# Kernel tuning notes

Measured on AMD Instinct MI355X. Metric: run time of the kernel, lower is better.

## Reference

```python
import jax, jax.numpy as jnp
import numpy as np

EMB = 1024
HEADS = 16
HEAD_DIM = EMB // HEADS
HIDDEN = 4096
EPS = 1e-05


def setup_inputs() -> dict:
    key = jax.random.key(0)
    ks = jax.random.split(key, 12)
    B, S = 2, 2048
    s_e = 1.0 / np.sqrt(EMB)
    s_h = 1.0 / np.sqrt(HIDDEN)
    return {
        "x": jax.random.normal(ks[0], (B, S, EMB), dtype=jnp.float32),
        "Wq": jax.random.normal(ks[1], (EMB, EMB), dtype=jnp.float32) * s_e,
        "Wk": jax.random.normal(ks[2], (EMB, EMB), dtype=jnp.float32) * s_e,
        "Wv": jax.random.normal(ks[3], (EMB, EMB), dtype=jnp.float32) * s_e,
        "Wo": jax.random.normal(ks[4], (EMB, EMB), dtype=jnp.float32) * s_e,
        "bo": jnp.zeros((EMB,), dtype=jnp.float32),
        "ln1_w": jnp.ones((EMB,), dtype=jnp.float32),
        "ln1_b": jnp.zeros((EMB,), dtype=jnp.float32),
        "ln2_w": jnp.ones((EMB,), dtype=jnp.float32),
        "ln2_b": jnp.zeros((EMB,), dtype=jnp.float32),
        "W1": jax.random.normal(ks[5], (EMB, HIDDEN), dtype=jnp.float32) * s_e,
        "b1": jnp.zeros((HIDDEN,), dtype=jnp.float32),
        "W2": jax.random.normal(ks[6], (HIDDEN, EMB), dtype=jnp.float32) * s_h,
        "b2": jnp.zeros((EMB,), dtype=jnp.float32),
    }


def _layernorm(x, w, b):
    mean = jnp.mean(x, axis=-1, keepdims=True)
    var = jnp.mean(jnp.square(x - mean), axis=-1, keepdims=True)
    return (x - mean) / jnp.sqrt(var + EPS) * w + b


def _attention(x, Wq, Wk, Wv, Wo, bo):
    B, S, E = x.shape
    # project and split heads: [B, H, S, D]
    def split(h):
        return h.reshape(B, S, HEADS, HEAD_DIM).transpose(0, 2, 1, 3)
    q = split(x @ Wq)
    k = split(x @ Wk)
    v = split(x @ Wv)
    scale = 1.0 / np.sqrt(HEAD_DIM)
    scores = jnp.einsum("bhqd,bhkd->bhqk", q, k) * scale
    causal = jnp.tril(jnp.ones((S, S), dtype=bool))
    scores = jnp.where(causal[None, None], scores, -jnp.inf)
    attn = jax.nn.softmax(scores, axis=-1)
    out = jnp.einsum("bhqk,bhkd->bhqd", attn, v)
    out = out.transpose(0, 2, 1, 3).reshape(B, S, E)
    return out @ Wo + bo


def reference(x, Wq, Wk, Wv, Wo, bo, ln1_w, ln1_b, ln2_w, ln2_b, W1, b1, W2, b2):
    h = x + _attention(_layernorm(x, ln1_w, ln1_b), Wq, Wk, Wv, Wo, bo)
    ff = jax.nn.relu(_layernorm(h, ln2_w, ln2_b) @ W1 + b1) @ W2 + b2
    return h + ff
```

## Files before the change

kernel.cpp:

```cpp
#include <hip/hip_runtime.h>

typedef unsigned short u16;
typedef unsigned int u32;
typedef __attribute__((ext_vector_type(8))) short s8v;
typedef __attribute__((ext_vector_type(4))) float f4v;

#define EMB 1024
#define SEQ 2048
#define BATCH 2
#define HEADS 16
#define HDIM 64
#define HID 4096
#define MROWS 4096

__device__ __forceinline__ float bf2f(u16 h) {
    u32 u = ((u32)h) << 16;
    union { u32 u; float f; } v; v.u = u; return v.f;
}
__device__ __forceinline__ u16 f2bf(float f) {
    union { float f; u32 u; } v; v.f = f;
    u32 r = v.u + 0x7FFFu + ((v.u >> 16) & 1u);
    return (u16)(r >> 16);
}
__device__ __forceinline__ float fexp2(float x) {
    float r; asm("v_exp_f32 %0, %1" : "=v"(r) : "v"(x)); return r;
}
__device__ __forceinline__ u32 cvtpk_bf16(float lo, float hi) {
    u32 r; asm("v_cvt_pk_bf16_f32 %0, %1, %2" : "=v"(r) : "v"(lo), "v"(hi)); return r;
}

__device__ __forceinline__ void gload16(const void* g, void* l) {
    __builtin_amdgcn_global_load_lds(
        (const __attribute__((address_space(1))) unsigned int*)g,
        (__attribute__((address_space(3))) unsigned int*)l, 16, 0, 0);
}

__global__ __launch_bounds__(256) void transpose_cast(const float* __restrict__ W,
                                                      u16* __restrict__ WT, int K, int N) {
    __shared__ float tile[32][33];
    int n0 = blockIdx.x * 32, k0 = blockIdx.y * 32;
    int tx = threadIdx.x, ty = threadIdx.y;
#pragma unroll
    for (int i = ty; i < 32; i += 8)
        tile[i][tx] = W[(size_t)(k0 + i) * N + n0 + tx];
    __syncthreads();
#pragma unroll
    for (int i = ty; i < 32; i += 8)
        WT[(size_t)(n0 + i) * K + k0 + tx] = f2bf(tile[tx][i]);
}

__global__ __launch_bounds__(256) void ln_kernel(const float* __restrict__ in,
                                                 const float* __restrict__ w,
                                                 const float* __restrict__ b,
                                                 u16* __restrict__ out) {
    const int row = blockIdx.x, t = threadIdx.x;
    const float4* rp = (const float4*)(in + (size_t)row * EMB);
    float4 v = rp[t];
    float s = v.x + v.y + v.z + v.w;
    __shared__ float red[4];
#pragma unroll
    for (int off = 32; off; off >>= 1) s += __shfl_xor(s, off);
    if ((t & 63) == 0) red[t >> 6] = s;
    __syncthreads();
    float mean = (red[0] + red[1] + red[2] + red[3]) * (1.f / EMB);
    float dx = v.x - mean, dy = v.y - mean, dz = v.z - mean, dw = v.w - mean;
    float ss = dx * dx + dy * dy + dz * dz + dw * dw;
#pragma unroll
    for (int off = 32; off; off >>= 1) ss += __shfl_xor(ss, off);
    __syncthreads();
    if ((t & 63) == 0) red[t >> 6] = ss;
    __syncthreads();
    float var = (red[0] + red[1] + red[2] + red[3]) * (1.f / EMB);
    float rstd = rsqrtf(var + 1e-5f);
    float4 wv = ((const float4*)w)[t];
    float4 bv = ((const float4*)b)[t];
    u16* op = out + (size_t)row * EMB + t * 4;
    op[0] = f2bf(dx * rstd * wv.x + bv.x);
    op[1] = f2bf(dy * rstd * wv.y + bv.y);
    op[2] = f2bf(dz * rstd * wv.z + bv.z);
    op[3] = f2bf(dw * rstd * wv.w + bv.w);
}

template <int EPI, int TM, int TN, int BK>
__global__ __launch_bounds__(256) void gemm_bt(const u16* __restrict__ A, const u16* __restrict__ BT,
                                               const float* __restrict__ bias, const float* res,
                                               void* outp, int M, int N, int K) {
    constexpr int S = BK / 8;
    constexpr int SM = S - 1;
    constexpr int MB_ = TM / 32;
    constexpr int NB = TN / 32;
    constexpr int KS = BK / 32;
    constexpr int ABUFB = TM * BK * 2;
    constexpr int BBUFB = TN * BK * 2;
    constexpr int ACH = (TM * S) / 256;
    constexpr int BCH = (TN * S) / 256;
    constexpr int PG = (MROWS / TM) / 8;
    __shared__ u16 As[2][TM * BK];
    __shared__ u16 Bs[2][TN * BK];
    const int t = threadIdx.x, w = t >> 6, lane = t & 63;
    const u32 id = blockIdx.x;
    const int xcd = (int)(id & 7), rem = (int)(id >> 3);
    const int by = xcd + (rem % PG) * 8;
    const int bx = rem / PG;
    const int m0 = by * TM, n0 = bx * TN;
    const int wr = w >> 1, wc = w & 1;
    const int la = lane & 15, lb = lane >> 4;
    f4v acc[MB_][NB] = {};

    const char* Ab = (const char*)A;
    const char* Bb = (const char*)BT;
    const size_t strideb = (size_t)K * 2;
    char* AsB = (char*)As;
    char* BsB = (char*)Bs;

    size_t asrc[ACH], bsrc[BCH];
#pragma unroll
    for (int i = 0; i < ACH; i++) {
        const int c = t + 256 * i, row = c / S, seg = c % S;
        asrc[i] = (size_t)(m0 + row) * strideb + (size_t)((seg ^ ((row >> 1) & SM)) * 16);
    }
#pragma unroll
    for (int i = 0; i < BCH; i++) {
        const int c = t + 256 * i, row = c / S, seg = c % S;
        bsrc[i] = (size_t)(n0 + row) * strideb + (size_t)((seg ^ ((row >> 1) & SM)) * 16);
    }

#pragma unroll
    for (int i = 0; i < ACH; i++) gload16(Ab + asrc[i], AsB + i * 4096 + w * 1024);
#pragma unroll
    for (int i = 0; i < BCH; i++) gload16(Bb + bsrc[i], BsB + i * 4096 + w * 1024);
    __syncthreads();

    int cur = 0;
    for (int k0 = 0; k0 < K; k0 += BK) {
        if (k0 + BK < K) {
            const size_t ko = (size_t)(k0 + BK) * 2;
            const int ab = (cur ^ 1) * ABUFB;
            const int bb = (cur ^ 1) * BBUFB;
#pragma unroll
            for (int i = 0; i < ACH; i++) gload16(Ab + asrc[i] + ko, AsB + ab + i * 4096 + w * 1024);
#pragma unroll
            for (int i = 0; i < BCH; i++) gload16(Bb + bsrc[i] + ko, BsB + bb + i * 4096 + w * 1024);
        }
#pragma unroll
        for (int ks = 0; ks < KS; ks++) {
            s8v a[MB_], bfr[NB];
#pragma unroll
            for (int mi = 0; mi < MB_; mi++) {
                const int row = wr * (TM / 2) + mi * 16 + la;
                const int sp = (ks * 4 + lb) ^ ((row >> 1) & SM);
                a[mi] = *(const s8v*)&As[cur][(row * S + sp) * 8];
            }
#pragma unroll
            for (int ni = 0; ni < NB; ni++) {
                const int row = wc * (TN / 2) + ni * 16 + la;
                const int sp = (ks * 4 + lb) ^ ((row >> 1) & SM);
                bfr[ni] = *(const s8v*)&Bs[cur][(row * S + sp) * 8];
            }
#pragma unroll
            for (int mi = 0; mi < MB_; mi++)
#pragma unroll
                for (int ni = 0; ni < NB; ni++)
                    acc[mi][ni] = __builtin_amdgcn_mfma_f32_16x16x32_bf16(a[mi], bfr[ni], acc[mi][ni], 0, 0, 0);
        }
        __syncthreads();
        cur ^= 1;
    }

    const int orow = m0 + wr * (TM / 2), ocol = n0 + wc * (TN / 2);
#pragma unroll
    for (int mi = 0; mi < MB_; mi++)
#pragma unroll
        for (int ni = 0; ni < NB; ni++)
#pragma unroll
            for (int j2 = 0; j2 < 4; j2++) {
                int r = orow + mi * 16 + lb * 4 + j2;
                int c = ocol + ni * 16 + la;
                float v = acc[mi][ni][j2];
                if (EPI == 0) {
                    ((u16*)outp)[(size_t)r * N + c] = f2bf(v);
                } else if (EPI == 1) {
                    ((float*)outp)[(size_t)r * N + c] = v + bias[c] + res[(size_t)r * N + c];
                } else {
                    v += bias[c];
                    ((u16*)outp)[(size_t)r * N + c] = f2bf(fmaxf(v, 0.f));
                }
            }
}

#define LDK 72
#define QKSCL 0.18033688f
__global__ __launch_bounds__(512) void fattn(const u16* __restrict__ QKV, u16* __restrict__ O) {
    const int t = threadIdx.x, w = t >> 6, lane = t & 63;
    const int la = lane & 15, lb = lane >> 4;
    const u32 id = blockIdx.x;
    const int bh = (int)((id & 7) * 4 + ((id >> 6) & 3));
    const int p = (int)((id >> 3) & 7);
    const int b = bh >> 4, h = bh & 15;

    __shared__ u16 K_lds[64 * LDK];
    __shared__ u16 Vt_lds[64 * LDK];
    __shared__ u16 P_lds[8][16 * LDK];

    const u16* base = QKV + (size_t)(b * SEQ) * 3072 + h * HDIM;
    const u16* Qg = base;
    const u16* Kg = base + 1024;
    const u16* Vg = base + 2048;
    u16* pw = &P_lds[w][0];

    const int krow = t >> 3, kseg = t & 7;
    const int vss = (t >> 5) & 7, vkp = t & 31;
    const bool vstager = (t < 256);

#pragma unroll
    for (int phase = 0; phase < 2; phase++) {
        const int qt = phase ? (15 - p) : p;
        const int qbase = qt * 128;
        const int nkv = 2 * qt + 2;
        const int wq0 = qbase + w * 16;

        s8v aq0, aq1;
        {
            const u16* qr = Qg + (size_t)(wq0 + la) * 3072 + lb * 8;
            aq0 = *(const s8v*)(qr);
            aq1 = *(const s8v*)(qr + 32);
        }
        float m[4], lp[4];
#pragma unroll
        for (int j = 0; j < 4; j++) { m[j] = -1e30f; lp[j] = 0.f; }
        f4v oacc[4] = {};

        s8v kstg, vstgA, vstgB;
        kstg = *(const s8v*)(Kg + (size_t)krow * 3072 + kseg * 8);
        if (vstager) {
            const u16* v0 = Vg + (size_t)(vkp * 2) * 3072 + vss * 8;
            vstgA = *(const s8v*)(v0);
            vstgB = *(const s8v*)(v0 + 3072);
        }

        for (int kt = 0; kt < nkv; ++kt) {
            const int kv0 = kt * 64;
            *(s8v*)&K_lds[krow * LDK + kseg * 8] = kstg;
            if (vstager) {
                u32* vt32 = (u32*)Vt_lds;
#pragma unroll
                for (int j2 = 0; j2 < 8; j2++)
                    vt32[(vss * 8 + j2) * (LDK / 2) + vkp] =
                        (u32)(u16)vstgA[j2] | ((u32)(u16)vstgB[j2] << 16);
            }
            if (kt + 1 < nkv) {
                const int nv0 = kv0 + 64;
                kstg = *(const s8v*)(Kg + (size_t)(nv0 + krow) * 3072 + kseg * 8);
                if (vstager) {
                    const u16* v0 = Vg + (size_t)(nv0 + vkp * 2) * 3072 + vss * 8;
                    vstgA = *(const s8v*)(v0);
                    vstgB = *(const s8v*)(v0 + 3072);
                }
            }
            __syncthreads();

            if (kv0 <= wq0 + 15) {
                f4v sacc[4] = {};
                __builtin_amdgcn_s_setprio(1);
#pragma unroll
                for (int kc = 0; kc < 4; kc++) {
                    s8v bk0 = *(const s8v*)&K_lds[(kc * 16 + la) * LDK + lb * 8];
                    s8v bk1 = *(const s8v*)&K_lds[(kc * 16 + la) * LDK + 32 + lb * 8];
                    sacc[kc] = __builtin_amdgcn_mfma_f32_16x16x32_bf16(aq0, bk0, sacc[kc], 0, 0, 0);
                    sacc[kc] = __builtin_amdgcn_mfma_f32_16x16x32_bf16(aq1, bk1, sacc[kc], 0, 0, 0);
                }
                __builtin_amdgcn_s_setprio(0);

                const bool doMask = (kv0 + 63 > wq0);
                float s[4][4];
                float mx[4];
                bool ok = true;
#pragma unroll
                for (int j = 0; j < 4; j++) {
                    const int row = wq0 + lb * 4 + j;
                    float s0 = sacc[0][j] * QKSCL;
                    float s1 = sacc[1][j] * QKSCL;
                    float s2 = sacc[2][j] * QKSCL;
                    float s3 = sacc[3][j] * QKSCL;
                    if (doMask) {
                        if (kv0 + 0 * 16 + la > row) s0 = -1e30f;
                        if (kv0 + 1 * 16 + la > row) s1 = -1e30f;
                        if (kv0 + 2 * 16 + la > row) s2 = -1e30f;
                        if (kv0 + 3 * 16 + la > row) s3 = -1e30f;
                    }
                    s[0][j] = s0; s[1][j] = s1; s[2][j] = s2; s[3][j] = s3;
                    float v = fmaxf(fmaxf(s0, s1), fmaxf(s2, s3));
                    mx[j] = v;
                    ok = ok && (v <= m[j] + 8.f);
                }
                if (__all(ok)) {
#pragma unroll
                    for (int j = 0; j < 4; j++) {
                        float e0 = fexp2(s[0][j] - m[j]);
                        float e1 = fexp2(s[1][j] - m[j]);
                        float e2 = fexp2(s[2][j] - m[j]);
                        float e3 = fexp2(s[3][j] - m[j]);
                        lp[j] += (e0 + e1) + (e2 + e3);
                        u32 c01 = cvtpk_bf16(e0, e1);
                        u32 c23 = cvtpk_bf16(e2, e3);
                        u16* pr = pw + (lb * 4 + j) * LDK + la;
                        pr[0]  = (u16)c01;
                        pr[16] = (u16)(c01 >> 16);
                        pr[32] = (u16)c23;
                        pr[48] = (u16)(c23 >> 16);
                    }
                } else {
#pragma unroll
                    for (int j = 0; j < 4; j++) {
                        float v = mx[j];
                        v = fmaxf(v, __shfl_xor(v, 1));
                        v = fmaxf(v, __shfl_xor(v, 2));
                        v = fmaxf(v, __shfl_xor(v, 4));
                        v = fmaxf(v, __shfl_xor(v, 8));
                        float mn = fmaxf(m[j], v);
                        float sc = fexp2(m[j] - mn);
                        m[j] = mn;
                        lp[j] *= sc;
#pragma unroll
                        for (int dt = 0; dt < 4; dt++) oacc[dt][j] *= sc;
                        float e0 = fexp2(s[0][j] - mn);
                        float e1 = fexp2(s[1][j] - mn);
                        float e2 = fexp2(s[2][j] - mn);
                        float e3 = fexp2(s[3][j] - mn);
                        lp[j] += (e0 + e1) + (e2 + e3);
                        u32 c01 = cvtpk_bf16(e0, e1);
                        u32 c23 = cvtpk_bf16(e2, e3);
                        u16* pr = pw + (lb * 4 + j) * LDK + la;
                        pr[0]  = (u16)c01;
                        pr[16] = (u16)(c01 >> 16);
                        pr[32] = (u16)c23;
                        pr[48] = (u16)(c23 >> 16);
                    }
                }

                s8v ap0 = *(const s8v*)&pw[la * LDK + lb * 8];
                s8v ap1 = *(const s8v*)&pw[la * LDK + 32 + lb * 8];
                __builtin_amdgcn_s_setprio(1);
#pragma unroll
                for (int dt = 0; dt < 4; dt++) {
                    s8v v0 = *(const s8v*)&Vt_lds[(dt * 16 + la) * LDK + lb * 8];
                    s8v v1 = *(const s8v*)&Vt_lds[(dt * 16 + la) * LDK + 32 + lb * 8];
                    oacc[dt] = __builtin_amdgcn_mfma_f32_16x16x32_bf16(ap0, v0, oacc[dt], 0, 0, 0);
                    oacc[dt] = __builtin_amdgcn_mfma_f32_16x16x32_bf16(ap1, v1, oacc[dt], 0, 0, 0);
                }
                __builtin_amdgcn_s_setprio(0);
            }
            __syncthreads();
        }

        float l[4];
#pragma unroll
        for (int j = 0; j < 4; j++) {
            float rs = lp[j];
            rs += __shfl_xor(rs, 1);
            rs += __shfl_xor(rs, 2);
            rs += __shfl_xor(rs, 4);
            rs += __shfl_xor(rs, 8);
            l[j] = rs;
        }
#pragma unroll
        for (int dt = 0; dt < 4; dt++) {
#pragma unroll
            for (int j = 0; j < 4; j++) {
                const int q = wq0 + lb * 4 + j;
                O[(size_t)(b * SEQ + q) * EMB + h * HDIM + dt * 16 + la] = f2bf(oacc[dt][j] / l[j]);
            }
        }
    }
}

extern "C" void kernel_launch(void* const* d_in, const int* in_sizes, int n_in,
                              void* d_out, int out_size, void* d_ws, size_t ws_size,
                              hipStream_t stream) {
    const float* x    = (const float*)d_in[0];
    const float* Wq   = (const float*)d_in[1];
    const float* Wk   = (const float*)d_in[2];
    const float* Wv   = (const float*)d_in[3];
    const float* Wo   = (const float*)d_in[4];
    const float* bo   = (const float*)d_in[5];
    const float* ln1w = (const float*)d_in[6];
    const float* ln1b = (const float*)d_in[7];
    const float* ln2w = (const float*)d_in[8];
    const float* ln2b = (const float*)d_in[9];
    const float* W1   = (const float*)d_in[10];
    const float* b1   = (const float*)d_in[11];
    const float* W2   = (const float*)d_in[12];
    const float* b2   = (const float*)d_in[13];

    const size_t MB = 1024 * 1024;
    char* ws = (char*)d_ws;
    u16* WqkvT = (u16*)(ws);
    u16* WoT   = (u16*)(ws + 6 * MB);
    u16* W1T   = (u16*)(ws + 8 * MB);
    u16* W2T   = (u16*)(ws + 16 * MB);
    u16* xn    = (u16*)(ws + 24 * MB);
    u16* QKV   = (u16*)(ws + 32 * MB);
    u16* mid   = (u16*)(ws + 32 * MB);
    u16* hn    = xn;
    float* hbuf = (float*)d_out;

    dim3 tb(32, 8);
    transpose_cast<<<dim3(32, 32), tb, 0, stream>>>(Wq, WqkvT, 1024, 1024);
    transpose_cast<<<dim3(32, 32), tb, 0, stream>>>(Wk, WqkvT + (size_t)1024 * 1024, 1024, 1024);
    transpose_cast<<<dim3(32, 32), tb, 0, stream>>>(Wv, WqkvT + (size_t)2048 * 1024, 1024, 1024);
    transpose_cast<<<dim3(32, 32), tb, 0, stream>>>(Wo, WoT, 1024, 1024);
    transpose_cast<<<dim3(128, 32), tb, 0, stream>>>(W1, W1T, 1024, 4096);
    transpose_cast<<<dim3(32, 128), tb, 0, stream>>>(W2, W2T, 4096, 1024);

    ln_kernel<<<MROWS, 256, 0, stream>>>(x, ln1w, ln1b, xn);

    gemm_bt<0, 128, 128, 32><<<dim3((3072 / 128) * (MROWS / 128)), 256, 0, stream>>>(
        xn, WqkvT, nullptr, nullptr, QKV, MROWS, 3072, 1024);

    fattn<<<dim3(256), 512, 0, stream>>>(QKV, xn);

    gemm_bt<1, 64, 64, 64><<<dim3((1024 / 64) * (MROWS / 64)), 256, 0, stream>>>(
        xn, WoT, bo, x, hbuf, MROWS, 1024, 1024);

    ln_kernel<<<MROWS, 256, 0, stream>>>(hbuf, ln2w, ln2b, hn);

    gemm_bt<2, 128, 128, 32><<<dim3((HID / 128) * (MROWS / 128)), 256, 0, stream>>>(
        hn, W1T, b1, nullptr, mid, MROWS, HID, 1024);

    gemm_bt<1, 64, 64, 64><<<dim3((1024 / 64) * (MROWS / 64)), 256, 0, stream>>>(
        mid, W2T, b2, hbuf, hbuf, MROWS, 1024, HID);
}
```

Before: 242.8 us.

## Widen flash-attention KV tile from 64 to 128 keys

Processes 128 keys per iteration instead of 64, with all 512 threads staging K and the transposed V. This halves the number of iterations and block-wide barriers and amortizes the softmax max/rescale bookkeeping over more keys. The cost is higher register pressure (8 score accumulators, 4 P fragments) and more LDS. Causal masking also becomes coarser, so warps near the diagonal do more wasted masked work.

```diff
diff --git a/kernel.cpp b/kernel.cpp
--- a/kernel.cpp
+++ b/kernel.cpp
@@ -189,6 +189,7 @@
 }
 
 #define LDK 72
+#define LDK2 136
 #define QKSCL 0.18033688f
 __global__ __launch_bounds__(512) void fattn(const u16* __restrict__ QKV, u16* __restrict__ O) {
     const int t = threadIdx.x, w = t >> 6, lane = t & 63;
@@ -198,9 +199,9 @@
     const int p = (int)((id >> 3) & 7);
     const int b = bh >> 4, h = bh & 15;
 
-    __shared__ u16 K_lds[64 * LDK];
-    __shared__ u16 Vt_lds[64 * LDK];
-    __shared__ u16 P_lds[8][16 * LDK];
+    __shared__ u16 K_lds[128 * LDK];
+    __shared__ u16 Vt_lds[64 * LDK2];
+    __shared__ u16 P_lds[8][16 * LDK2];
 
     const u16* base = QKV + (size_t)(b * SEQ) * 3072 + h * HDIM;
     const u16* Qg = base;
@@ -208,15 +209,14 @@
     const u16* Vg = base + 2048;
     u16* pw = &P_lds[w][0];
 
-    const int krow = t >> 3, kseg = t & 7;
-    const int vss = (t >> 5) & 7, vkp = t & 31;
-    const bool vstager = (t < 256);
+    const int krow = t >> 2, ks4 = t & 3;
+    const int vkp = t & 63, vss = t >> 6;
 
 #pragma unroll
     for (int phase = 0; phase < 2; phase++) {
         const int qt = phase ? (15 - p) : p;
         const int qbase = qt * 128;
-        const int nkv = 2 * qt + 2;
+        const int nkv = qt + 1;
         const int wq0 = qbase + w * 16;
 
         s8v aq0, aq1;
@@ -230,40 +230,43 @@
         for (int j = 0; j < 4; j++) { m[j] = -1e30f; lp[j] = 0.f; }
         f4v oacc[4] = {};
 
-        s8v kstg, vstgA, vstgB;
-        kstg = *(const s8v*)(Kg + (size_t)krow * 3072 + kseg * 8);
-        if (vstager) {
+        s8v kstgA, kstgB, vstgA, vstgB;
+        {
+            const u16* kr = Kg + (size_t)krow * 3072;
+            kstgA = *(const s8v*)(kr + ks4 * 8);
+            kstgB = *(const s8v*)(kr + (ks4 + 4) * 8);
             const u16* v0 = Vg + (size_t)(vkp * 2) * 3072 + vss * 8;
             vstgA = *(const s8v*)(v0);
             vstgB = *(const s8v*)(v0 + 3072);
         }
 
         for (int kt = 0; kt < nkv; ++kt) {
-            const int kv0 = kt * 64;
-            *(s8v*)&K_lds[krow * LDK + kseg * 8] = kstg;
-            if (vstager) {
+            const int kv0 = kt * 128;
+            *(s8v*)&K_lds[krow * LDK + ks4 * 8] = kstgA;
+            *(s8v*)&K_lds[krow * LDK + (ks4 + 4) * 8] = kstgB;
+            {
                 u32* vt32 = (u32*)Vt_lds;
 #pragma unroll
                 for (int j2 = 0; j2 < 8; j2++)
-                    vt32[(vss * 8 + j2) * (LDK / 2) + vkp] =
+                    vt32[(vss * 8 + j2) * (LDK2 / 2) + vkp] =
                         (u32)(u16)vstgA[j2] | ((u32)(u16)vstgB[j2] << 16);
             }
             if (kt + 1 < nkv) {
-                const int nv0 = kv0 + 64;
-                kstg = *(const s8v*)(Kg + (size_t)(nv0 + krow) * 3072 + kseg * 8);
-                if (vstager) {
-                    const u16* v0 = Vg + (size_t)(nv0 + vkp * 2) * 3072 + vss * 8;
-                    vstgA = *(const s8v*)(v0);
-                    vstgB = *(const s8v*)(v0 + 3072);
-                }
+                const int nv0 = kv0 + 128;
+                const u16* kr = Kg + (size_t)(nv0 + krow) * 3072;
+                kstgA = *(const s8v*)(kr + ks4 * 8);
+                kstgB = *(const s8v*)(kr + (ks4 + 4) * 8);
+                const u16* v0 = Vg + (size_t)(nv0 + vkp * 2) * 3072 + vss * 8;
+                vstgA = *(const s8v*)(v0);
+                vstgB = *(const s8v*)(v0 + 3072);
             }
             __syncthreads();
 
             if (kv0 <= wq0 + 15) {
-                f4v sacc[4] = {};
+                f4v sacc[8] = {};
                 __builtin_amdgcn_s_setprio(1);
 #pragma unroll
-                for (int kc = 0; kc < 4; kc++) {
+                for (int kc = 0; kc < 8; kc++) {
                     s8v bk0 = *(const s8v*)&K_lds[(kc * 16 + la) * LDK + lb * 8];
                     s8v bk1 = *(const s8v*)&K_lds[(kc * 16 + la) * LDK + 32 + lb * 8];
                     sacc[kc] = __builtin_amdgcn_mfma_f32_16x16x32_bf16(aq0, bk0, sacc[kc], 0, 0, 0);
@@ -271,43 +274,42 @@
                 }
                 __builtin_amdgcn_s_setprio(0);
 
-                const bool doMask = (kv0 + 63 > wq0);
-                float s[4][4];
+                const bool doMask = (kv0 + 127 > wq0);
+                float s[8][4];
                 float mx[4];
                 bool ok = true;
 #pragma unroll
                 for (int j = 0; j < 4; j++) {
                     const int row = wq0 + lb * 4 + j;
-                    float s0 = sacc[0][j] * QKSCL;
-                    float s1 = sacc[1][j] * QKSCL;
-                    float s2 = sacc[2][j] * QKSCL;
-                    float s3 = sacc[3][j] * QKSCL;
-                    if (doMask) {
-                        if (kv0 + 0 * 16 + la > row) s0 = -1e30f;
-                        if (kv0 + 1 * 16 + la > row) s1 = -1e30f;
-                        if (kv0 + 2 * 16 + la > row) s2 = -1e30f;
-                        if (kv0 + 3 * 16 + la > row) s3 = -1e30f;
+                    float v = -1e30f;
+#pragma unroll
+                    for (int kc = 0; kc < 8; kc++) {
+                        float sv = sacc[kc][j] * QKSCL;
+                        if (doMask && (kv0 + kc * 16 + la > row)) sv = -1e30f;
+                        s[kc][j] = sv;
+                        v = fmaxf(v, sv);
                     }
-                    s[0][j] = s0; s[1][j] = s1; s[2][j] = s2; s[3][j] = s3;
-                    float v = fmaxf(fmaxf(s0, s1), fmaxf(s2, s3));
                     mx[j] = v;
                     ok = ok && (v <= m[j] + 8.f);
                 }
                 if (__all(ok)) {
 #pragma unroll
                     for (int j = 0; j < 4; j++) {
-                        float e0 = fexp2(s[0][j] - m[j]);
-                        float e1 = fexp2(s[1][j] - m[j]);
-                        float e2 = fexp2(s[2][j] - m[j]);
-                        float e3 = fexp2(s[3][j] - m[j]);
-                        lp[j] += (e0 + e1) + (e2 + e3);
-                        u32 c01 = cvtpk_bf16(e0, e1);
-                        u32 c23 = cvtpk_bf16(e2, e3);
-                        u16* pr = pw + (lb * 4 + j) * LDK + la;
-                        pr[0]  = (u16)c01;
-                        pr[16] = (u16)(c01 >> 16);
-                        pr[32] = (u16)c23;
-                        pr[48] = (u16)(c23 >> 16);
+                        float e[8];
+                        float rs = 0.f;
+#pragma unroll
+                        for (int kc = 0; kc < 8; kc++) {
+                            e[kc] = fexp2(s[kc][j] - m[j]);
+                            rs += e[kc];
+                        }
+                        lp[j] += rs;
+                        u16* pr = pw + (lb * 4 + j) * LDK2 + la;
+#pragma unroll
+                        for (int kc = 0; kc < 8; kc += 2) {
+                            u32 c2 = cvtpk_bf16(e[kc], e[kc + 1]);
+                            pr[kc * 16] = (u16)c2;
+                            pr[(kc + 1) * 16] = (u16)(c2 >> 16);
+                        }
                     }
                 } else {
 #pragma unroll
@@ -323,30 +325,36 @@
                         lp[j] *= sc;
 #pragma unroll
                         for (int dt = 0; dt < 4; dt++) oacc[dt][j] *= sc;
-                        float e0 = fexp2(s[0][j] - mn);
-                        float e1 = fexp2(s[1][j] - mn);
-                        float e2 = fexp2(s[2][j] - mn);
-                        float e3 = fexp2(s[3][j] - mn);
-                        lp[j] += (e0 + e1) + (e2 + e3);
-                        u32 c01 = cvtpk_bf16(e0, e1);
-                        u32 c23 = cvtpk_bf16(e2, e3);
-                        u16* pr = pw + (lb * 4 + j) * LDK + la;
-                        pr[0]  = (u16)c01;
-                        pr[16] = (u16)(c01 >> 16);
-                        pr[32] = (u16)c23;
-                        pr[48] = (u16)(c23 >> 16);
+                        float e[8];
+                        float rs = 0.f;
+#pragma unroll
+                        for (int kc = 0; kc < 8; kc++) {
+                            e[kc] = fexp2(s[kc][j] - mn);
+                            rs += e[kc];
+                        }
+                        lp[j] += rs;
+                        u16* pr = pw + (lb * 4 + j) * LDK2 + la;
+#pragma unroll
+                        for (int kc = 0; kc < 8; kc += 2) {
+                            u32 c2 = cvtpk_bf16(e[kc], e[kc + 1]);
+                            pr[kc * 16] = (u16)c2;
+                            pr[(kc + 1) * 16] = (u16)(c2 >> 16);
+                        }
                     }
                 }
 
-                s8v ap0 = *(const s8v*)&pw[la * LDK + lb * 8];
-                s8v ap1 = *(const s8v*)&pw[la * LDK + 32 + lb * 8];
+                s8v ap[4];
+#pragma unroll
+                for (int ks = 0; ks < 4; ks++)
+                    ap[ks] = *(const s8v*)&pw[la * LDK2 + ks * 32 + lb * 8];
                 __builtin_amdgcn_s_setprio(1);
 #pragma unroll
                 for (int dt = 0; dt < 4; dt++) {
-                    s8v v0 = *(const s8v*)&Vt_lds[(dt * 16 + la) * LDK + lb * 8];
-                    s8v v1 = *(const s8v*)&Vt_lds[(dt * 16 + la) * LDK + 32 + lb * 8];
-                    oacc[dt] = __builtin_amdgcn_mfma_f32_16x16x32_bf16(ap0, v0, oacc[dt], 0, 0, 0);
-                    oacc[dt] = __builtin_amdgcn_mfma_f32_16x16x32_bf16(ap1, v1, oacc[dt], 0, 0, 0);
+#pragma unroll
+                    for (int ks = 0; ks < 4; ks++) {
+                        s8v v0 = *(const s8v*)&Vt_lds[(dt * 16 + la) * LDK2 + ks * 32 + lb * 8];
+                        oacc[dt] = __builtin_amdgcn_mfma_f32_16x16x32_bf16(ap[ks], v0, oacc[dt], 0, 0, 0);
+                    }
                 }
                 __builtin_amdgcn_s_setprio(0);
             }
```

New measurement: 251.1 us. +3.4%, slower.
